# Kernel optimization log

Hardware: AMD Instinct MI355X
Metric: run time of the kernel (lower is better)

Reference implementation:

```python
import jax, jax.numpy as jnp
import numpy as np

DIM = 1024
CTX_DIM = 768
HEADS = 16
D_HEAD = 64
INNER = HEADS * D_HEAD  # 1024
EPS = 1e-5


def _layernorm(x, g, b):
    mu = jnp.mean(x, axis=-1, keepdims=True)
    var = jnp.mean(jnp.square(x - mu), axis=-1, keepdims=True)
    return (x - mu) * jax.lax.rsqrt(var + EPS) * g + b


def setup_inputs() -> dict:
    key = jax.random.key(0)
    ks = jax.random.split(key, 8)
    s = lambda fan_in: 1.0 / np.sqrt(fan_in)
    return {
        "x": jax.random.normal(ks[0], (4, 2048, DIM), dtype=jnp.float32),
        "context": jax.random.normal(ks[1], (4, 2048, CTX_DIM), dtype=jnp.float32),
        "norm_g": jnp.ones((DIM,), jnp.float32),
        "norm_b": jnp.zeros((DIM,), jnp.float32),
        "normc_g": jnp.ones((CTX_DIM,), jnp.float32),
        "normc_b": jnp.zeros((CTX_DIM,), jnp.float32),
        # Linear weights stored [in, out] so y = x @ W (bias=False as in module)
        "Wq": jax.random.uniform(ks[2], (DIM, INNER), jnp.float32, -s(DIM), s(DIM)),
        "Wk": jax.random.uniform(ks[3], (CTX_DIM, INNER), jnp.float32, -s(CTX_DIM), s(CTX_DIM)),
        "Wv": jax.random.uniform(ks[4], (CTX_DIM, INNER), jnp.float32, -s(CTX_DIM), s(CTX_DIM)),
        "Wo": jax.random.uniform(ks[5], (INNER, DIM), jnp.float32, -s(INNER), s(INNER)),
    }


def reference(x, context, norm_g, norm_b, normc_g, normc_b, Wq, Wk, Wv, Wo):
    b, n, _ = x.shape
    m = context.shape[1]
    xn = _layernorm(x, norm_g, norm_b)
    cn = _layernorm(context, normc_g, normc_b)
    # project and split heads: b n (h d) -> b h n d
    split = lambda t, L: t.reshape(b, L, HEADS, D_HEAD).transpose(0, 2, 1, 3)
    q = split(xn @ Wq, n)
    k = split(cn @ Wk, m)
    v = split(cn @ Wv, m)
    sim = jnp.einsum('bhid,bhjd->bhij', q, k) / np.sqrt(D_HEAD)
    attn = jax.nn.softmax(sim, axis=-1)  # dropout p=0 (eval): identity
    out = jnp.einsum('bhij,bhjd->bhid', attn, v)
    out = out.transpose(0, 2, 1, 3).reshape(b, n, INNER)
    return out @ Wo
```

## Files before the change

kernel.cpp:

```cpp
#include <hip/hip_runtime.h>
#include <hip/hip_bf16.h>
#include <stdint.h>

#define TOK 8192
#define NQ 2048
#define DIMX 1024
#define CTXD 768

typedef __attribute__((ext_vector_type(8))) short short8;
typedef __attribute__((ext_vector_type(4))) float f32x4;
typedef __attribute__((ext_vector_type(2))) unsigned int u32x2;

typedef __attribute__((address_space(3))) uint32_t lds_u32_t;
typedef const __attribute__((address_space(1))) uint32_t glb_u32_t;

__device__ __forceinline__ void gld_lds16(const void* g, void* l) {
  __builtin_amdgcn_global_load_lds((glb_u32_t*)g, (lds_u32_t*)l, 16, 0, 0);
}

__device__ __forceinline__ uint16_t f2bf(float f) {
  union { float f; uint32_t u; } v; v.f = f;
  uint32_t r = v.u + 0x7fffu + ((v.u >> 16) & 1u);
  return (uint16_t)(r >> 16);
}

__device__ __forceinline__ uint32_t cvt_pk_bf16(float lo, float hi) {
  uint32_t d;
  asm("v_cvt_pk_bf16_f32 %0, %1, %2" : "=v"(d) : "v"(lo), "v"(hi));
  return d;
}

__device__ __forceinline__ float fexp2(float x) {
#if __has_builtin(__builtin_amdgcn_exp2f)
  return __builtin_amdgcn_exp2f(x);
#else
  float d;
  asm volatile("v_exp_f32 %0, %1\n\ts_nop 1" : "=v"(d) : "v"(x));
  return d;
#endif
}

__global__ __launch_bounds__(256)
void ln_both_kernel(const float* __restrict__ x, const float* __restrict__ gx,
                    const float* __restrict__ bx,
                    const float* __restrict__ c, const float* __restrict__ gc,
                    const float* __restrict__ bc,
                    uint16_t* __restrict__ xn, uint16_t* __restrict__ cn) {
  int row = blockIdx.x;
  int tid = threadIdx.x;
  const float *src, *g, *bb; uint16_t* dst; int COLS;
  if (row < TOK) { src = x; g = gx; bb = bx; dst = xn; COLS = DIMX; }
  else { row -= TOK; src = c; g = gc; bb = bc; dst = cn; COLS = CTXD; }
  bool act = tid * 4 < COLS;
  float4 v = make_float4(0.f, 0.f, 0.f, 0.f);
  if (act) v = *(const float4*)(src + (size_t)row * COLS + tid * 4);
  float s1 = v.x + v.y + v.z + v.w;
  float s2 = v.x*v.x + v.y*v.y + v.z*v.z + v.w*v.w;
#pragma unroll
  for (int off = 1; off < 64; off <<= 1) {
    s1 += __shfl_xor(s1, off);
    s2 += __shfl_xor(s2, off);
  }
  __shared__ float sm[2][4];
  int w = tid >> 6;
  if ((tid & 63) == 0) { sm[0][w] = s1; sm[1][w] = s2; }
  __syncthreads();
  float t1 = sm[0][0] + sm[0][1] + sm[0][2] + sm[0][3];
  float t2 = sm[1][0] + sm[1][1] + sm[1][2] + sm[1][3];
  float mu = t1 / COLS;
  float var = t2 / COLS - mu * mu;
  float rs = rsqrtf(var + 1e-5f);
  if (act) {
    float4 gv = *(const float4*)(g + tid * 4);
    float4 bv = *(const float4*)(bb + tid * 4);
    uint32_t lo = (uint32_t)f2bf((v.x - mu) * rs * gv.x + bv.x) |
                  ((uint32_t)f2bf((v.y - mu) * rs * gv.y + bv.y) << 16);
    uint32_t hi = (uint32_t)f2bf((v.z - mu) * rs * gv.z + bv.z) |
                  ((uint32_t)f2bf((v.w - mu) * rs * gv.w + bv.w) << 16);
    uint2 o; o.x = lo; o.y = hi;
    *(uint2*)(dst + (size_t)row * COLS + tid * 4) = o;
  }
}

__global__ __launch_bounds__(256)
void transpose_cast4_kernel(const float* __restrict__ W0, const float* __restrict__ W1,
                            const float* __restrict__ W2, const float* __restrict__ W3,
                            uint16_t* __restrict__ T0, uint16_t* __restrict__ T1,
                            uint16_t* __restrict__ T2, uint16_t* __restrict__ T3) {
  int z = blockIdx.z;
  const float* W = (z == 0) ? W0 : (z == 1) ? W1 : (z == 2) ? W2 : W3;
  uint16_t* WT   = (z == 0) ? T0 : (z == 1) ? T1 : (z == 2) ? T2 : T3;
  int K = (z == 1 || z == 2) ? CTXD : DIMX;
  const int N = DIMX;
  int c0 = blockIdx.x * 32, r0 = blockIdx.y * 32;
  if (r0 >= K) return;
  __shared__ float t[32][33];
  int tx = threadIdx.x & 31, ty = threadIdx.x >> 5;
#pragma unroll
  for (int i = 0; i < 4; i++)
    t[ty + 8*i][tx] = W[(size_t)(r0 + ty + 8*i) * N + c0 + tx];
  __syncthreads();
#pragma unroll
  for (int i = 0; i < 4; i++)
    WT[(size_t)(c0 + ty + 8*i) * K + r0 + tx] = f2bf(t[tx][ty + 8*i]);
}

__device__ __forceinline__ void gemm_block(
    const uint16_t* __restrict__ A, const uint16_t* __restrict__ BT,
    void* __restrict__ C, int N, int K, float oscale,
    int out_bf16, int permc, int m0, int n0,
    uint16_t* Al, uint16_t* Bl, int tid) {
  int l = tid & 63, w = tid >> 6;
  int g = l >> 4, r = l & 15;
  int wm = w >> 1, wn = w & 1;
  f32x4 acc[4][4] = {};
  int srow = tid >> 3, sslot = tid & 7;

  for (int kt = 0; kt < K; kt += 64) {
    __syncthreads();
#pragma unroll
    for (int c = 0; c < 4; c++) {
      int row = c * 32 + srow;
      int ksrc = (sslot * 8) ^ ((row & 7) << 3);
      gld_lds16(A + (size_t)(m0 + row) * K + kt + ksrc, Al + (c * 256 + w * 64) * 8);
    }
#pragma unroll
    for (int c = 0; c < 4; c++) {
      int row = c * 32 + srow;
      int ksrc = (sslot * 8) ^ ((row & 7) << 3);
      gld_lds16(BT + (size_t)(n0 + row) * K + kt + ksrc, Bl + (c * 256 + w * 64) * 8);
    }
    __syncthreads();
#pragma unroll
    for (int kk = 0; kk < 2; kk++) {
      int kb2 = (kk * 32 + g * 8) * 2;
      short8 af[4], bfr[4];
#pragma unroll
      for (int mf = 0; mf < 4; mf++) {
        int row = wm * 64 + mf * 16 + r;
        af[mf] = *(const short8*)((const char*)Al + row * 128 + (kb2 ^ ((row & 7) << 4)));
      }
#pragma unroll
      for (int nf = 0; nf < 4; nf++) {
        int row = wn * 64 + nf * 16 + r;
        bfr[nf] = *(const short8*)((const char*)Bl + row * 128 + (kb2 ^ ((row & 7) << 4)));
      }
#pragma unroll
      for (int mf = 0; mf < 4; mf++)
#pragma unroll
        for (int nf = 0; nf < 4; nf++)
          acc[mf][nf] = __builtin_amdgcn_mfma_f32_16x16x32_bf16(af[mf], bfr[nf], acc[mf][nf], 0, 0, 0);
    }
  }
#pragma unroll
  for (int mf = 0; mf < 4; mf++) {
#pragma unroll
    for (int i = 0; i < 4; i++) {
      size_t row = (size_t)m0 + wm * 64 + mf * 16 + g * 4 + i;
      if (permc) {
        int pbase = ((r >> 3) << 4) | (((r >> 2) & 1) << 3) | (r & 3);
        uint16_t* cb = (uint16_t*)C + row * N + n0 + wn * 64;
        cb[pbase +  0] = f2bf(acc[mf][0][i]);
        cb[pbase +  4] = f2bf(acc[mf][1][i]);
        cb[pbase + 32] = f2bf(acc[mf][2][i]);
        cb[pbase + 36] = f2bf(acc[mf][3][i]);
      } else {
#pragma unroll
        for (int nf = 0; nf < 4; nf++) {
          int col = n0 + wn * 64 + nf * 16 + r;
          float val = acc[mf][nf][i] * oscale;
          if (out_bf16) ((uint16_t*)C)[row * N + col] = f2bf(val);
          else          ((float*)C)[row * N + col] = val;
        }
      }
    }
  }
}

__global__ __launch_bounds__(256)
void gemm_proj3_kernel(const uint16_t* __restrict__ xn, const uint16_t* __restrict__ cn,
                       const uint16_t* __restrict__ WqT, const uint16_t* __restrict__ WkT,
                       const uint16_t* __restrict__ WvT,
                       uint16_t* __restrict__ Qs, uint16_t* __restrict__ Ks,
                       uint16_t* __restrict__ VTs, float qscale) {
  __shared__ __align__(16) uint16_t Al[128 * 64];
  __shared__ __align__(16) uint16_t Bl[128 * 64];
  int flat = blockIdx.x;
  flat = (flat & 7) * 192 + (flat >> 3);
  const uint16_t* A; const uint16_t* BT; uint16_t* C;
  int N, K, permc, m0, n0;
  float osc = 1.f;
  if (flat < 512) {
    A = xn; BT = WqT; C = Qs; N = DIMX; K = DIMX; permc = 0; osc = qscale;
    n0 = (flat & 7) * 128; m0 = (flat >> 3) * 128;
  } else if (flat < 1024) {
    int f = flat - 512;
    A = cn; BT = WkT; C = Ks; N = DIMX; K = CTXD; permc = 0;
    n0 = (f & 7) * 128; m0 = (f >> 3) * 128;
  } else {
    int f = flat - 1024;
    A = WvT; BT = cn; C = VTs; N = TOK; K = CTXD; permc = 1;
    n0 = (f & 63) * 128; m0 = (f >> 6) * 128;
  }
  gemm_block(A, BT, C, N, K, osc, 1, permc, m0, n0, Al, Bl, threadIdx.x);
}

__global__ __launch_bounds__(256)
void gemm_out_kernel(const uint16_t* __restrict__ A, const uint16_t* __restrict__ BT,
                     float* __restrict__ C, int M, int N, int K) {
  __shared__ __align__(16) uint16_t Al[128 * 64];
  __shared__ __align__(16) uint16_t Bl[128 * 64];
  int flat = blockIdx.y * gridDim.x + blockIdx.x;
  int nwg = gridDim.x * gridDim.y;
  flat = (flat & 7) * (nwg >> 3) + (flat >> 3);
  int bx = flat & (gridDim.x - 1);
  int by = flat / gridDim.x;
  gemm_block(A, BT, C, N, K, 1.f, 0, 0, by * 128, bx * 128, Al, Bl, threadIdx.x);
}

__global__ __launch_bounds__(256)
void attn_kernel(const uint16_t* __restrict__ Q, const uint16_t* __restrict__ Kp,
                 const uint16_t* __restrict__ VT, uint16_t* __restrict__ O) {
  __shared__ __align__(16) uint16_t Kl[64 * 64];
  __shared__ __align__(16) uint16_t Vl[64 * 64];
  int tid = threadIdx.x;
  int l = tid & 63, w = tid >> 6;
  int g = l >> 4, r = l & 15;
  int flat = blockIdx.y * 16 + blockIdx.x;
  flat = (flat & 7) * 128 + (flat >> 3);
  int q0 = (flat & 15) * 128;
  int bh = flat >> 4, b = bh >> 4, h = bh & 15;

  short8 qa[2][2];
#pragma unroll
  for (int qb = 0; qb < 2; qb++) {
    const uint16_t* qptr = Q + (size_t)(b * NQ + q0 + w * 32 + qb * 16 + r) * DIMX + h * 64;
    qa[qb][0] = *(const short8*)(qptr + g * 8);
    qa[qb][1] = *(const short8*)(qptr + 32 + g * 8);
  }

  float lpart[2] = {0.f, 0.f};
  f32x4 oacc[2][4] = {};

  const uint16_t* kbase = Kp + (size_t)(b * NQ) * DIMX + h * 64;
  const uint16_t* vbase = VT + (size_t)(h * 64) * TOK + b * NQ;
  int srow = tid >> 3, sslot = tid & 7;

  for (int kv0 = 0; kv0 < NQ; kv0 += 64) {
    __syncthreads();
#pragma unroll
    for (int c = 0; c < 2; c++) {
      int key = c * 32 + srow;
      int dsrc = (sslot * 8) ^ ((key & 7) << 3);
      gld_lds16(kbase + (size_t)(kv0 + key) * DIMX + dsrc, Kl + (c * 256 + w * 64) * 8);
    }
#pragma unroll
    for (int c = 0; c < 2; c++) {
      int d = c * 32 + srow;
      int ksrc = (sslot * 8) ^ ((d & 7) << 3);
      gld_lds16(vbase + (size_t)d * TOK + kv0 + ksrc, Vl + (c * 256 + w * 64) * 8);
    }
    __syncthreads();

    f32x4 sc[2][4] = {};
    __builtin_amdgcn_s_setprio(1);
#pragma unroll
    for (int kk = 0; kk < 2; kk++) {
      int kb2 = (kk * 32 + g * 8) * 2;
#pragma unroll
      for (int c = 0; c < 4; c++) {
        int row = c * 16 + r;
        short8 kf = *(const short8*)((const char*)Kl + row * 128 + (kb2 ^ ((row & 7) << 4)));
        sc[0][c] = __builtin_amdgcn_mfma_f32_16x16x32_bf16(kf, qa[0][kk], sc[0][c], 0, 0, 0);
        sc[1][c] = __builtin_amdgcn_mfma_f32_16x16x32_bf16(kf, qa[1][kk], sc[1][c], 0, 0, 0);
      }
    }
    __builtin_amdgcn_s_setprio(0);

    short8 pa[2][2];
#pragma unroll
    for (int qb = 0; qb < 2; qb++) {
      float pe[4][4];
#pragma unroll
      for (int c = 0; c < 4; c++)
#pragma unroll
        for (int i = 0; i < 4; i++) {
          pe[c][i] = fexp2(sc[qb][c][i]);
          lpart[qb] += pe[c][i];
        }
#pragma unroll
      for (int kk = 0; kk < 2; kk++) {
        union { uint32_t u[4]; short8 s; } pk;
        pk.u[0] = cvt_pk_bf16(pe[kk * 2][0], pe[kk * 2][1]);
        pk.u[1] = cvt_pk_bf16(pe[kk * 2][2], pe[kk * 2][3]);
        pk.u[2] = cvt_pk_bf16(pe[kk * 2 + 1][0], pe[kk * 2 + 1][1]);
        pk.u[3] = cvt_pk_bf16(pe[kk * 2 + 1][2], pe[kk * 2 + 1][3]);
        pa[qb][kk] = pk.s;
      }
    }

    __builtin_amdgcn_s_setprio(1);
#pragma unroll
    for (int kk = 0; kk < 2; kk++) {
#pragma unroll
      for (int c = 0; c < 4; c++) {
        int row = c * 16 + r;
        short8 vf = *(const short8*)((const char*)Vl + row * 128 + (((kk * 32 + g * 8) * 2) ^ ((row & 7) << 4)));
        oacc[0][c] = __builtin_amdgcn_mfma_f32_16x16x32_bf16(pa[0][kk], vf, oacc[0][c], 0, 0, 0);
        oacc[1][c] = __builtin_amdgcn_mfma_f32_16x16x32_bf16(pa[1][kk], vf, oacc[1][c], 0, 0, 0);
      }
    }
    __builtin_amdgcn_s_setprio(0);
  }

#pragma unroll
  for (int qb = 0; qb < 2; qb++) {
    lpart[qb] += __shfl_xor(lpart[qb], 16);
    lpart[qb] += __shfl_xor(lpart[qb], 32);
  }

#pragma unroll
  for (int qb = 0; qb < 2; qb++) {
    uint16_t* obase = O + (size_t)(b * NQ + q0 + w * 32 + qb * 16) * DIMX + h * 64;
#pragma unroll
    for (int i = 0; i < 4; i++) {
      float li = __shfl(lpart[qb], g * 4 + i);
      float inv = 1.f / li;
#pragma unroll
      for (int c = 0; c < 4; c++)
        obase[(size_t)(g * 4 + i) * DIMX + c * 16 + r] = f2bf(oacc[qb][c][i] * inv);
    }
  }
}

extern "C" void kernel_launch(void* const* d_in, const int* in_sizes, int n_in,
                              void* d_out, int out_size, void* d_ws, size_t ws_size,
                              hipStream_t stream) {
  (void)in_sizes; (void)n_in; (void)out_size; (void)ws_size;
  const float* x       = (const float*)d_in[0];
  const float* ctx     = (const float*)d_in[1];
  const float* norm_g  = (const float*)d_in[2];
  const float* norm_b  = (const float*)d_in[3];
  const float* normc_g = (const float*)d_in[4];
  const float* normc_b = (const float*)d_in[5];
  const float* Wq      = (const float*)d_in[6];
  const float* Wk      = (const float*)d_in[7];
  const float* Wv      = (const float*)d_in[8];
  const float* Wo      = (const float*)d_in[9];

  char* p = (char*)d_ws;
  uint16_t* xn  = (uint16_t*)p; p += (size_t)TOK * DIMX * 2;
  uint16_t* cn  = (uint16_t*)p; p += (size_t)TOK * CTXD * 2;
  uint16_t* WqT = (uint16_t*)p; p += (size_t)DIMX * DIMX * 2;
  uint16_t* WkT = (uint16_t*)p; p += (size_t)DIMX * CTXD * 2;
  uint16_t* WvT = (uint16_t*)p; p += (size_t)DIMX * CTXD * 2;
  uint16_t* WoT = (uint16_t*)p; p += (size_t)DIMX * DIMX * 2;
  uint16_t* Qs  = (uint16_t*)p; p += (size_t)TOK * DIMX * 2;
  uint16_t* Ks  = (uint16_t*)p; p += (size_t)TOK * DIMX * 2;
  uint16_t* VTs = (uint16_t*)p; p += (size_t)DIMX * TOK * 2;
  uint16_t* AO  = (uint16_t*)p; p += (size_t)TOK * DIMX * 2;

  ln_both_kernel<<<TOK * 2, 256, 0, stream>>>(x, norm_g, norm_b, ctx, normc_g, normc_b, xn, cn);

  transpose_cast4_kernel<<<dim3(DIMX/32, DIMX/32, 4), 256, 0, stream>>>(
      Wq, Wk, Wv, Wo, WqT, WkT, WvT, WoT);

  const float qscale = 0.125f * 1.44269504088896340736f;
  gemm_proj3_kernel<<<1536, 256, 0, stream>>>(xn, cn, WqT, WkT, WvT, Qs, Ks, VTs, qscale);

  attn_kernel<<<dim3(NQ/128, 64), 256, 0, stream>>>(Qs, Ks, VTs, AO);

  gemm_out_kernel<<<dim3(DIMX/128, TOK/128), 256, 0, stream>>>(AO, WoT, (float*)d_out, TOK, DIMX, DIMX);
}
```

Measured before the change: 199.6 us.

## Merge layernorm and weight transpose launches; enlarge attention query tile

The layernorm and weight transpose/cast kernels are merged into one launch, with the extra blocks handling the transposes. This removes one kernel launch and lets the two independent jobs overlap. The attention kernel now processes 256 queries per block (64 per wave) instead of 128, so each K/V tile loaded into LDS is reused across twice as many queries. The cost is more accumulator registers, a launch bound requesting 2 blocks per SM, and half as many blocks (512), which may hurt occupancy or raise register pressure.

```diff
diff --git a/kernel.cpp b/kernel.cpp
--- a/kernel.cpp
+++ b/kernel.cpp
@@ -41,13 +41,38 @@
 }
 
 __global__ __launch_bounds__(256)
-void ln_both_kernel(const float* __restrict__ x, const float* __restrict__ gx,
-                    const float* __restrict__ bx,
-                    const float* __restrict__ c, const float* __restrict__ gc,
-                    const float* __restrict__ bc,
-                    uint16_t* __restrict__ xn, uint16_t* __restrict__ cn) {
-  int row = blockIdx.x;
+void ln_tr_kernel(const float* __restrict__ x, const float* __restrict__ gx,
+                  const float* __restrict__ bx,
+                  const float* __restrict__ c, const float* __restrict__ gc,
+                  const float* __restrict__ bc,
+                  uint16_t* __restrict__ xn, uint16_t* __restrict__ cn,
+                  const float* __restrict__ W0, const float* __restrict__ W1,
+                  const float* __restrict__ W2, const float* __restrict__ W3,
+                  uint16_t* __restrict__ T0, uint16_t* __restrict__ T1,
+                  uint16_t* __restrict__ T2, uint16_t* __restrict__ T3) {
+  int bid = blockIdx.x;
   int tid = threadIdx.x;
+  if (bid >= 2 * TOK) {
+    int t = bid - 2 * TOK;
+    int z = t >> 10, rem = t & 1023;
+    const float* W = (z == 0) ? W0 : (z == 1) ? W1 : (z == 2) ? W2 : W3;
+    uint16_t* WT   = (z == 0) ? T0 : (z == 1) ? T1 : (z == 2) ? T2 : T3;
+    int K = (z == 1 || z == 2) ? CTXD : DIMX;
+    const int N = DIMX;
+    int c0 = (rem & 31) * 32, r0 = (rem >> 5) * 32;
+    if (r0 >= K) return;
+    __shared__ float tb[32][33];
+    int tx = tid & 31, ty = tid >> 5;
+#pragma unroll
+    for (int i = 0; i < 4; i++)
+      tb[ty + 8*i][tx] = W[(size_t)(r0 + ty + 8*i) * N + c0 + tx];
+    __syncthreads();
+#pragma unroll
+    for (int i = 0; i < 4; i++)
+      WT[(size_t)(c0 + ty + 8*i) * K + r0 + tx] = f2bf(tb[tx][ty + 8*i]);
+    return;
+  }
+  int row = bid;
   const float *src, *g, *bb; uint16_t* dst; int COLS;
   if (row < TOK) { src = x; g = gx; bb = bx; dst = xn; COLS = DIMX; }
   else { row -= TOK; src = c; g = gc; bb = bc; dst = cn; COLS = CTXD; }
@@ -80,29 +105,6 @@
     uint2 o; o.x = lo; o.y = hi;
     *(uint2*)(dst + (size_t)row * COLS + tid * 4) = o;
   }
-}
-
-__global__ __launch_bounds__(256)
-void transpose_cast4_kernel(const float* __restrict__ W0, const float* __restrict__ W1,
-                            const float* __restrict__ W2, const float* __restrict__ W3,
-                            uint16_t* __restrict__ T0, uint16_t* __restrict__ T1,
-                            uint16_t* __restrict__ T2, uint16_t* __restrict__ T3) {
-  int z = blockIdx.z;
-  const float* W = (z == 0) ? W0 : (z == 1) ? W1 : (z == 2) ? W2 : W3;
-  uint16_t* WT   = (z == 0) ? T0 : (z == 1) ? T1 : (z == 2) ? T2 : T3;
-  int K = (z == 1 || z == 2) ? CTXD : DIMX;
-  const int N = DIMX;
-  int c0 = blockIdx.x * 32, r0 = blockIdx.y * 32;
-  if (r0 >= K) return;
-  __shared__ float t[32][33];
-  int tx = threadIdx.x & 31, ty = threadIdx.x >> 5;
-#pragma unroll
-  for (int i = 0; i < 4; i++)
-    t[ty + 8*i][tx] = W[(size_t)(r0 + ty + 8*i) * N + c0 + tx];
-  __syncthreads();
-#pragma unroll
-  for (int i = 0; i < 4; i++)
-    WT[(size_t)(c0 + ty + 8*i) * K + r0 + tx] = f2bf(t[tx][ty + 8*i]);
 }
 
 __device__ __forceinline__ void gemm_block(
@@ -218,7 +220,7 @@
   gemm_block(A, BT, C, N, K, 1.f, 0, 0, by * 128, bx * 128, Al, Bl, threadIdx.x);
 }
 
-__global__ __launch_bounds__(256)
+__global__ __launch_bounds__(256, 2)
 void attn_kernel(const uint16_t* __restrict__ Q, const uint16_t* __restrict__ Kp,
                  const uint16_t* __restrict__ VT, uint16_t* __restrict__ O) {
   __shared__ __align__(16) uint16_t Kl[64 * 64];
@@ -226,21 +228,21 @@
   int tid = threadIdx.x;
   int l = tid & 63, w = tid >> 6;
   int g = l >> 4, r = l & 15;
-  int flat = blockIdx.y * 16 + blockIdx.x;
-  flat = (flat & 7) * 128 + (flat >> 3);
-  int q0 = (flat & 15) * 128;
-  int bh = flat >> 4, b = bh >> 4, h = bh & 15;
-
-  short8 qa[2][2];
-#pragma unroll
-  for (int qb = 0; qb < 2; qb++) {
-    const uint16_t* qptr = Q + (size_t)(b * NQ + q0 + w * 32 + qb * 16 + r) * DIMX + h * 64;
+  int flat = blockIdx.y * 8 + blockIdx.x;
+  flat = (flat & 7) * 64 + (flat >> 3);
+  int q0 = (flat & 7) * 256;
+  int bh = flat >> 3, b = bh >> 4, h = bh & 15;
+
+  short8 qa[4][2];
+#pragma unroll
+  for (int qb = 0; qb < 4; qb++) {
+    const uint16_t* qptr = Q + (size_t)(b * NQ + q0 + w * 64 + qb * 16 + r) * DIMX + h * 64;
     qa[qb][0] = *(const short8*)(qptr + g * 8);
     qa[qb][1] = *(const short8*)(qptr + 32 + g * 8);
   }
 
-  float lpart[2] = {0.f, 0.f};
-  f32x4 oacc[2][4] = {};
+  float lpart[4] = {0.f, 0.f, 0.f, 0.f};
+  f32x4 oacc[4][4] = {};
 
   const uint16_t* kbase = Kp + (size_t)(b * NQ) * DIMX + h * 64;
   const uint16_t* vbase = VT + (size_t)(h * 64) * TOK + b * NQ;
@@ -262,7 +264,7 @@
     }
     __syncthreads();
 
-    f32x4 sc[2][4] = {};
+    f32x4 sc[4][4] = {};
     __builtin_amdgcn_s_setprio(1);
 #pragma unroll
     for (int kk = 0; kk < 2; kk++) {
@@ -271,15 +273,16 @@
       for (int c = 0; c < 4; c++) {
         int row = c * 16 + r;
         short8 kf = *(const short8*)((const char*)Kl + row * 128 + (kb2 ^ ((row & 7) << 4)));
-        sc[0][c] = __builtin_amdgcn_mfma_f32_16x16x32_bf16(kf, qa[0][kk], sc[0][c], 0, 0, 0);
-        sc[1][c] = __builtin_amdgcn_mfma_f32_16x16x32_bf16(kf, qa[1][kk], sc[1][c], 0, 0, 0);
+#pragma unroll
+        for (int qb = 0; qb < 4; qb++)
+          sc[qb][c] = __builtin_amdgcn_mfma_f32_16x16x32_bf16(kf, qa[qb][kk], sc[qb][c], 0, 0, 0);
       }
     }
     __builtin_amdgcn_s_setprio(0);
 
-    short8 pa[2][2];
-#pragma unroll
-    for (int qb = 0; qb < 2; qb++) {
+    short8 pa[4][2];
+#pragma unroll
+    for (int qb = 0; qb < 4; qb++) {
       float pe[4][4];
 #pragma unroll
       for (int c = 0; c < 4; c++)
@@ -306,22 +309,23 @@
       for (int c = 0; c < 4; c++) {
         int row = c * 16 + r;
         short8 vf = *(const short8*)((const char*)Vl + row * 128 + (((kk * 32 + g * 8) * 2) ^ ((row & 7) << 4)));
-        oacc[0][c] = __builtin_amdgcn_mfma_f32_16x16x32_bf16(pa[0][kk], vf, oacc[0][c], 0, 0, 0);
-        oacc[1][c] = __builtin_amdgcn_mfma_f32_16x16x32_bf16(pa[1][kk], vf, oacc[1][c], 0, 0, 0);
+#pragma unroll
+        for (int qb = 0; qb < 4; qb++)
+          oacc[qb][c] = __builtin_amdgcn_mfma_f32_16x16x32_bf16(pa[qb][kk], vf, oacc[qb][c], 0, 0, 0);
       }
     }
     __builtin_amdgcn_s_setprio(0);
   }
 
 #pragma unroll
-  for (int qb = 0; qb < 2; qb++) {
+  for (int qb = 0; qb < 4; qb++) {
     lpart[qb] += __shfl_xor(lpart[qb], 16);
     lpart[qb] += __shfl_xor(lpart[qb], 32);
   }
 
 #pragma unroll
-  for (int qb = 0; qb < 2; qb++) {
-    uint16_t* obase = O + (size_t)(b * NQ + q0 + w * 32 + qb * 16) * DIMX + h * 64;
+  for (int qb = 0; qb < 4; qb++) {
+    uint16_t* obase = O + (size_t)(b * NQ + q0 + w * 64 + qb * 16) * DIMX + h * 64;
 #pragma unroll
     for (int i = 0; i < 4; i++) {
       float li = __shfl(lpart[qb], g * 4 + i);
@@ -360,15 +364,14 @@
   uint16_t* VTs = (uint16_t*)p; p += (size_t)DIMX * TOK * 2;
   uint16_t* AO  = (uint16_t*)p; p += (size_t)TOK * DIMX * 2;
 
-  ln_both_kernel<<<TOK * 2, 256, 0, stream>>>(x, norm_g, norm_b, ctx, normc_g, normc_b, xn, cn);
-
-  transpose_cast4_kernel<<<dim3(DIMX/32, DIMX/32, 4), 256, 0, stream>>>(
+  ln_tr_kernel<<<2 * TOK + 4096, 256, 0, stream>>>(
+      x, norm_g, norm_b, ctx, normc_g, normc_b, xn, cn,
       Wq, Wk, Wv, Wo, WqT, WkT, WvT, WoT);
 
   const float qscale = 0.125f * 1.44269504088896340736f;
   gemm_proj3_kernel<<<1536, 256, 0, stream>>>(xn, cn, WqT, WkT, WvT, Qs, Ks, VTs, qscale);
 
-  attn_kernel<<<dim3(NQ/128, 64), 256, 0, stream>>>(Qs, Ks, VTs, AO);
+  attn_kernel<<<dim3(8, 64), 256, 0, stream>>>(Qs, Ks, VTs, AO);
 
   gemm_out_kernel<<<dim3(DIMX/128, TOK/128), 256, 0, stream>>>(AO, WoT, (float*)d_out, TOK, DIMX, DIMX);
 }
```

New measurement: 178.2 us, median of 2. -10.7%, faster.
